# Optimization experiments

Hardware: AMD Instinct MI355X
Metric: run time of the kernel (lower is better)

## Reference

```python
import jax, jax.numpy as jnp
import numpy as np

T, B, D, O = 2048, 32, 512, 512


def setup_inputs() -> dict:
    key = jax.random.key(0)
    ks = jax.random.split(key, 12)
    s = 0.02
    return {
        "word": jax.random.normal(ks[0], (T, B, D), dtype=jnp.float32),
        "Wf": jax.random.normal(ks[1], (D, D), dtype=jnp.float32) * s,
        "bf": jax.random.normal(ks[2], (D,), dtype=jnp.float32) * s,
        "Wi": jax.random.normal(ks[3], (D, D), dtype=jnp.float32) * s,
        "bi": jax.random.normal(ks[4], (D,), dtype=jnp.float32) * s,
        "Wz": jax.random.normal(ks[5], (D, D), dtype=jnp.float32) * s,
        "bz": jax.random.normal(ks[6], (D,), dtype=jnp.float32) * s,
        "Wo": jax.random.normal(ks[7], (D, D), dtype=jnp.float32) * s,
        "bo": jax.random.normal(ks[8], (D,), dtype=jnp.float32) * s,
        "Wy": jax.random.normal(ks[9], (O, D), dtype=jnp.float32) * s,
        "by": jax.random.normal(ks[10], (O,), dtype=jnp.float32) * s,
    }


def reference(word, Wf, bf, Wi, bi, Wz, bz, Wo, bo, Wy, by):
    # Faithful to the original buggy module:
    #  - forward discards the updated cell state, so c == 0 every step and
    #    the zf gate (wf) never affects the output.
    #  - z and zo reuse wi(hidden) instead of wz/wo(hidden).
    #  - the same Linear is applied to letter and hidden, so bias is doubled
    #    in zi (and zf).
    Bsz, Dd = word.shape[1], word.shape[2]

    def step(h, x):  # h: [B, D], x: [B, D]
        hWi = h @ Wi.T                                  # reused by zi, z, zo
        zi = jax.nn.sigmoid(x @ Wi.T + hWi + 2.0 * bi)
        z = jax.nn.sigmoid(x @ Wz.T + bz + hWi + bi)
        zo = jax.nn.sigmoid(x @ Wo.T + bo + hWi + bi)
        c = zi * z                                      # zf * 0 + zi * z
        h_new = zo * jnp.tanh(c)
        return h_new, None

    h0 = jnp.zeros((Bsz, Dd), dtype=word.dtype)
    h_final, _ = jax.lax.scan(step, h0, word)
    # original computes wy(hidden) every step but only returns the last one
    output = h_final @ Wy.T + by                        # [B, O]
    return output
```

## Files before the change

### kernel.cpp

```cpp
#include <hip/hip_runtime.h>

typedef unsigned int u32;
typedef unsigned short u16;
typedef unsigned long long u64;
typedef _Float16 f16;
typedef f16 f16x2 __attribute__((ext_vector_type(2)));

__device__ __forceinline__ float fdot2(u32 a, u32 b, float c) {
#if __has_builtin(__builtin_amdgcn_fdot2)
    return __builtin_amdgcn_fdot2(__builtin_bit_cast(f16x2, a),
                                  __builtin_bit_cast(f16x2, b), c, false);
#else
    f16x2 av = __builtin_bit_cast(f16x2, a), bv = __builtin_bit_cast(f16x2, b);
    c += (float)av[0] * (float)bv[0];
    c += (float)av[1] * (float)bv[1];
    return c;
#endif
}

__device__ __forceinline__ u32 pack2h(float a, float b) {
    f16x2 h; h[0] = (f16)a; h[1] = (f16)b;
    return __builtin_bit_cast(u32, h);
}
__device__ __forceinline__ float h2f(u16 x) { return (float)__builtin_bit_cast(f16, x); }
__device__ __forceinline__ u16 f2h(float x) { f16 h = (f16)x; return __builtin_bit_cast(u16, h); }

__device__ __forceinline__ float fexp(float x) {
#if __has_builtin(__builtin_amdgcn_exp2f)
    return __builtin_amdgcn_exp2f(x * 1.44269504088896f);
#else
    return __expf(x);
#endif
}
__device__ __forceinline__ float frcp(float x) {
#if __has_builtin(__builtin_amdgcn_rcpf)
    return __builtin_amdgcn_rcpf(x);
#else
    return 1.0f / x;
#endif
}
__device__ __forceinline__ float fsigmoid(float x) { return frcp(1.0f + fexp(-x)); }
__device__ __forceinline__ float ftanh_pos(float x) { return 1.0f - 2.0f * frcp(fexp(2.0f * x) + 1.0f); }

__device__ __forceinline__ u64 load_l2(const u64* p) {
    u64 v;
    asm volatile("global_load_dwordx2 %0, %1, off sc0\n\ts_waitcnt vmcnt(0)"
                 : "=v"(v) : "v"(p) : "memory");
    return v;
}
__device__ __forceinline__ void store_l2(u64* p, u64 v) {
    asm volatile("global_store_dwordx2 %0, %1, off sc0" :: "v"(p), "v"(v) : "memory");
}

__global__ __launch_bounds__(256) void k0_pack(const float* __restrict__ Wi,
                                               const float* __restrict__ Wy,
                                               u32* __restrict__ WpkT,
                                               u32* __restrict__ Wypk) {
    const int bx = blockIdx.x, tid = threadIdx.x;
    if (bx < 512) {
        const float2 v = *(const float2*)(Wi + (size_t)bx * 512 + 2 * tid);
        WpkT[(size_t)bx * 256 + tid] = pack2h(v.x, v.y);
    } else {
        const int p = bx - 512;
        #pragma unroll
        for (int r = 0; r < 2; ++r) {
            const int d = tid + 256 * r;
            Wypk[(size_t)p * 512 + d] =
                pack2h(Wy[(size_t)d * 512 + 2 * p], Wy[(size_t)d * 512 + 2 * p + 1]);
        }
    }
}

__global__ __launch_bounds__(256) void k1_gates(
    const float* __restrict__ word,
    const float* __restrict__ Wi, const float* __restrict__ Wz, const float* __restrict__ Wo,
    const float* __restrict__ bi, const float* __restrict__ bz, const float* __restrict__ bo,
    u16* __restrict__ Xi, u16* __restrict__ Xz, u16* __restrict__ Xo)
{
    __shared__ uint4 ws2v[3][128][4];
    __shared__ u32 xs2[2][16][36];

    const int tid = threadIdx.x;
    const int d_l = tid & 63;
    const int bq  = tid >> 6;
    const int t0  = blockIdx.x * 2;
    const int d0  = blockIdx.y * 128;

    const float* Wg[3] = {Wi, Wz, Wo};

    float acc[2][2][8][3];
    #pragma unroll
    for (int tt = 0; tt < 2; ++tt)
        #pragma unroll
        for (int db = 0; db < 2; ++db)
            #pragma unroll
            for (int j = 0; j < 8; ++j)
                #pragma unroll
                for (int g = 0; g < 3; ++g) acc[tt][db][j][g] = 0.0f;

    for (int k0c = 0; k0c < 512; k0c += 32) {
        {
            const int p = tid & 15, bg = tid >> 4;
            #pragma unroll
            for (int tt = 0; tt < 2; ++tt)
                #pragma unroll
                for (int j = 0; j < 2; ++j) {
                    const int bb = bg * 2 + j;
                    const float2 v = *(const float2*)(word + (((size_t)(t0 + tt) * 32 + bb) * 512 + k0c + 2 * p));
                    xs2[tt][p][bb] = pack2h(v.x, v.y);
                }
        }
        {
            #pragma unroll
            for (int cc = 0; cc < 6; ++cc) {
                const int c = tid + 256 * cc;
                const int g = c >> 9, r = c & 511, pg = r >> 7, i = r & 127;
                const float* src = Wg[g] + (size_t)(d0 + i) * 512 + k0c + 8 * pg;
                const float4 v0 = ((const float4*)src)[0];
                const float4 v1 = ((const float4*)src)[1];
                uint4 cell;
                cell.x = pack2h(v0.x, v0.y); cell.y = pack2h(v0.z, v0.w);
                cell.z = pack2h(v1.x, v1.y); cell.w = pack2h(v1.z, v1.w);
                ws2v[g][i][(pg + (i >> 2)) & 3] = cell;
            }
        }
        __syncthreads();
        #pragma unroll
        for (int pg = 0; pg < 4; ++pg) {
            uint4 wc[3][2];
            #pragma unroll
            for (int g = 0; g < 3; ++g)
                #pragma unroll
                for (int db = 0; db < 2; ++db) {
                    const int d = d_l + 64 * db;
                    wc[g][db] = ws2v[g][d][(pg + (d >> 2)) & 3];
                }
            #pragma unroll
            for (int p = 0; p < 4; ++p) {
                const int pair = 4 * pg + p;
                u32 x2[2][8];
                #pragma unroll
                for (int tt = 0; tt < 2; ++tt) {
                    const uint4* xr = (const uint4*)&xs2[tt][pair][bq * 8];
                    uint4 xa = xr[0], xb = xr[1];
                    x2[tt][0] = xa.x; x2[tt][1] = xa.y; x2[tt][2] = xa.z; x2[tt][3] = xa.w;
                    x2[tt][4] = xb.x; x2[tt][5] = xb.y; x2[tt][6] = xb.z; x2[tt][7] = xb.w;
                }
                u32 w[3][2];
                #pragma unroll
                for (int g = 0; g < 3; ++g)
                    #pragma unroll
                    for (int db = 0; db < 2; ++db) {
                        const uint4 v = wc[g][db];
                        w[g][db] = (p == 0) ? v.x : (p == 1) ? v.y : (p == 2) ? v.z : v.w;
                    }
                #pragma unroll
                for (int tt = 0; tt < 2; ++tt)
                    #pragma unroll
                    for (int db = 0; db < 2; ++db)
                        #pragma unroll
                        for (int j = 0; j < 8; ++j)
                            #pragma unroll
                            for (int g = 0; g < 3; ++g)
                                acc[tt][db][j][g] = fdot2(x2[tt][j], w[g][db], acc[tt][db][j][g]);
            }
        }
        __syncthreads();
    }

    #pragma unroll
    for (int db = 0; db < 2; ++db) {
        const int d = d0 + 64 * db + d_l;
        const float b0 = 2.0f * bi[d];
        const float b1 = bz[d] + bi[d];
        const float b2 = bo[d] + bi[d];
        #pragma unroll
        for (int tt = 0; tt < 2; ++tt)
            #pragma unroll
            for (int j = 0; j < 8; ++j) {
                const size_t o = ((size_t)(t0 + tt) * 32 + (bq * 8 + j)) * 512 + d;
                Xi[o] = f2h(acc[tt][db][j][0] + b0);
                Xz[o] = f2h(acc[tt][db][j][1] + b1);
                Xo[o] = f2h(acc[tt][db][j][2] + b2);
            }
    }
}

__global__ __launch_bounds__(512, 2) void k2_recur(
    const u16* __restrict__ Xi, const u16* __restrict__ Xz, const u16* __restrict__ Xo,
    const u32* __restrict__ WpkT, const u32* __restrict__ Wypk,
    u64* __restrict__ exchF, u64* __restrict__ exchS,
    const float* __restrict__ by, float* __restrict__ out)
{
    __shared__ alignas(16) u16 hb[2][256];
    __shared__ alignas(16) u16 hfull[512];

    const int bid  = blockIdx.x;
    const int half = (bid >> 3) & 1;
    const int b    = (bid & 7) | ((bid >> 4) << 3);
    const int tid  = threadIdx.x;

    const uint4* WpkT4 = (const uint4*)WpkT;
    u32 wq[128];
    #pragma unroll
    for (int i = 0; i < 32; ++i) {
        const uint4 v = WpkT4[(size_t)tid * 64 + half * 32 + i];
        wq[4 * i + 0] = v.x; wq[4 * i + 1] = v.y;
        wq[4 * i + 2] = v.z; wq[4 * i + 3] = v.w;
    }
    #pragma unroll
    for (int i = 0; i < 128; ++i) asm volatile("" : "+v"(wq[i]));

    if (tid < 256) hb[0][tid] = (u16)0;
    __syncthreads();

    const size_t me  = (size_t)(b * 2 + half) * 2 * 512 + tid;
    const size_t pa  = (size_t)(b * 2 + (half ^ 1)) * 2 * 512 + tid;
    u64* eoF = exchF + me;  u64* eoS = exchS + me;
    const u64* eiF = exchF + pa;  const u64* eiS = exchS + pa;

    const int ownhalf = ((tid >> 8) == half);
    const int hloc = tid & 255;

    u16 xi_c = Xi[(size_t)b * 512 + tid];
    u16 xz_c = Xz[(size_t)b * 512 + tid];
    u16 xo_c = Xo[(size_t)b * 512 + tid];

    float hn = 0.0f;
    for (int t = 0; t < 2048; ++t) {
        const int par = t & 1;
        const int tn = (t + 1) & 2047;
        const size_t xb = ((size_t)tn * 32 + b) * 512 + tid;
        const u16 xi_n = Xi[xb], xz_n = Xz[xb], xo_n = Xo[xb];

        const uint4* hv = (const uint4*)&hb[par][0];
        float a0 = 0.f, a1 = 0.f, a2 = 0.f, a3 = 0.f;
        #pragma unroll
        for (int i = 0; i < 32; ++i) {
            const uint4 hc = hv[i];
            a0 = fdot2(hc.x, wq[4 * i + 0], a0);
            a1 = fdot2(hc.y, wq[4 * i + 1], a1);
            a2 = fdot2(hc.z, wq[4 * i + 2], a2);
            a3 = fdot2(hc.w, wq[4 * i + 3], a3);
        }
        const float p = (a0 + a1) + (a2 + a3);

        const u32 tag = (u32)(t + 1);
        const u64 msg = ((u64)tag << 32) | (u64)__builtin_bit_cast(u32, p);
        store_l2(eoF + (size_t)par * 512, msg);
        __hip_atomic_store(eoS + (size_t)par * 512, msg,
                           __ATOMIC_RELAXED, __HIP_MEMORY_SCOPE_AGENT);

        u64 m;
        for (;;) {
            m = load_l2(eiF + (size_t)par * 512);
            if ((u32)(m >> 32) == tag) break;
            m = __hip_atomic_load(eiS + (size_t)par * 512,
                                  __ATOMIC_RELAXED, __HIP_MEMORY_SCOPE_AGENT);
            if ((u32)(m >> 32) == tag) break;
        }
        const float v = p + __builtin_bit_cast(float, (u32)m);

        const float zi = fsigmoid(h2f(xi_c) + v);
        const float z  = fsigmoid(h2f(xz_c) + v);
        const float zo = fsigmoid(h2f(xo_c) + v);
        hn = zo * ftanh_pos(zi * z);

        if (ownhalf) hb[par ^ 1][hloc] = f2h(hn);
        __syncthreads();

        xi_c = xi_n; xz_c = xz_n; xo_c = xo_n;
    }

    hfull[tid] = f2h(hn);
    __syncthreads();
    {
        const uint4* hv = (const uint4*)&hfull[0];
        float e0 = 0.f, e1 = 0.f, e2 = 0.f, e3 = 0.f;
        #pragma unroll 8
        for (int i = 0; i < 64; ++i) {
            const uint4 hc = hv[i];
            e0 = fdot2(hc.x, Wypk[(size_t)(4 * i + 0) * 512 + tid], e0);
            e1 = fdot2(hc.y, Wypk[(size_t)(4 * i + 1) * 512 + tid], e1);
            e2 = fdot2(hc.z, Wypk[(size_t)(4 * i + 2) * 512 + tid], e2);
            e3 = fdot2(hc.w, Wypk[(size_t)(4 * i + 3) * 512 + tid], e3);
        }
        out[(size_t)b * 512 + tid] = (e0 + e1) + (e2 + e3) + by[tid];
    }
}

extern "C" void kernel_launch(void* const* d_in, const int* in_sizes, int n_in,
                              void* d_out, int out_size, void* d_ws, size_t ws_size,
                              hipStream_t stream) {
    const float* word = (const float*)d_in[0];
    const float* Wi = (const float*)d_in[3];
    const float* bi = (const float*)d_in[4];
    const float* Wz = (const float*)d_in[5];
    const float* bz = (const float*)d_in[6];
    const float* Wo = (const float*)d_in[7];
    const float* bo = (const float*)d_in[8];
    const float* Wy = (const float*)d_in[9];
    const float* by = (const float*)d_in[10];
    float* out = (float*)d_out;

    char* ws = (char*)d_ws;
    const size_t XN = (size_t)2048 * 32 * 512 * sizeof(u16);
    u16* Xi = (u16*)(ws);
    u16* Xz = (u16*)(ws + XN);
    u16* Xo = (u16*)(ws + 2 * XN);
    u32* WpkT  = (u32*)(ws + 3 * XN);
    u32* Wypk  = (u32*)(ws + 3 * XN + (size_t)524288);
    u64* exchF = (u64*)(ws + 3 * XN + (size_t)2 * 524288);
    u64* exchS = (u64*)(ws + 3 * XN + (size_t)3 * 524288);

    k0_pack<<<768, 256, 0, stream>>>(Wi, Wy, WpkT, Wypk);

    dim3 g1(1024, 4);
    k1_gates<<<g1, 256, 0, stream>>>(word, Wi, Wz, Wo, bi, bz, bo, Xi, Xz, Xo);

    k2_recur<<<64, 512, 0, stream>>>(Xi, Xz, Xo, WpkT, Wypk, exchF, exchS, by, out);
}
```

Baseline: 4.270 ms.

## Merge split recurrence blocks into one 1024-thread block with shared-memory exchange

Each batch element's recurrence now runs in a single 1024-thread workgroup, with the two halves of the K-reduction exchanging partial sums through LDS and barriers. Previously two workgroups on different CUs exchanged them through L2 with tagged spin-polling every timestep. This removes cross-CU global synchronization latency on the serial critical path. The cost is half the CUs in use, an extra barrier per step, and heavy register pressure from 128 weight registers per thread at 1024 threads.

Result: slower. 9.763 ms (+128.6%).

```diff
diff --git a/kernel.cpp b/kernel.cpp
--- a/kernel.cpp
+++ b/kernel.cpp
@@ -41,16 +41,6 @@
 }
 __device__ __forceinline__ float fsigmoid(float x) { return frcp(1.0f + fexp(-x)); }
 __device__ __forceinline__ float ftanh_pos(float x) { return 1.0f - 2.0f * frcp(fexp(2.0f * x) + 1.0f); }
-
-__device__ __forceinline__ u64 load_l2(const u64* p) {
-    u64 v;
-    asm volatile("global_load_dwordx2 %0, %1, off sc0\n\ts_waitcnt vmcnt(0)"
-                 : "=v"(v) : "v"(p) : "memory");
-    return v;
-}
-__device__ __forceinline__ void store_l2(u64* p, u64 v) {
-    asm volatile("global_store_dwordx2 %0, %1, off sc0" :: "v"(p), "v"(v) : "memory");
-}
 
 __global__ __launch_bounds__(256) void k0_pack(const float* __restrict__ Wi,
                                                const float* __restrict__ Wy,
@@ -186,54 +176,52 @@
     }
 }
 
-__global__ __launch_bounds__(512, 2) void k2_recur(
+__global__ __launch_bounds__(1024, 1) void k2_recur(
     const u16* __restrict__ Xi, const u16* __restrict__ Xz, const u16* __restrict__ Xo,
     const u32* __restrict__ WpkT, const u32* __restrict__ Wypk,
-    u64* __restrict__ exchF, u64* __restrict__ exchS,
     const float* __restrict__ by, float* __restrict__ out)
 {
-    __shared__ alignas(16) u16 hb[2][256];
-    __shared__ alignas(16) u16 hfull[512];
-
-    const int bid  = blockIdx.x;
-    const int half = (bid >> 3) & 1;
-    const int b    = (bid & 7) | ((bid >> 4) << 3);
+    __shared__ alignas(16) u16 hb[2][512];
+    __shared__ float pbuf[512];
+
+    const int b    = blockIdx.x;
     const int tid  = threadIdx.x;
+    const int half = tid >> 9;
+    const int d    = tid & 511;
 
     const uint4* WpkT4 = (const uint4*)WpkT;
     u32 wq[128];
     #pragma unroll
     for (int i = 0; i < 32; ++i) {
-        const uint4 v = WpkT4[(size_t)tid * 64 + half * 32 + i];
+        const uint4 v = WpkT4[(size_t)d * 64 + half * 32 + i];
         wq[4 * i + 0] = v.x; wq[4 * i + 1] = v.y;
         wq[4 * i + 2] = v.z; wq[4 * i + 3] = v.w;
     }
     #pragma unroll
     for (int i = 0; i < 128; ++i) asm volatile("" : "+v"(wq[i]));
 
-    if (tid < 256) hb[0][tid] = (u16)0;
+    if (tid < 512) hb[0][tid] = (u16)0;
     __syncthreads();
 
-    const size_t me  = (size_t)(b * 2 + half) * 2 * 512 + tid;
-    const size_t pa  = (size_t)(b * 2 + (half ^ 1)) * 2 * 512 + tid;
-    u64* eoF = exchF + me;  u64* eoS = exchS + me;
-    const u64* eiF = exchF + pa;  const u64* eiS = exchS + pa;
-
-    const int ownhalf = ((tid >> 8) == half);
-    const int hloc = tid & 255;
-
-    u16 xi_c = Xi[(size_t)b * 512 + tid];
-    u16 xz_c = Xz[(size_t)b * 512 + tid];
-    u16 xo_c = Xo[(size_t)b * 512 + tid];
+    u16 xi_c = 0, xz_c = 0, xo_c = 0;
+    if (half == 0) {
+        xi_c = Xi[(size_t)b * 512 + d];
+        xz_c = Xz[(size_t)b * 512 + d];
+        xo_c = Xo[(size_t)b * 512 + d];
+    }
 
     float hn = 0.0f;
     for (int t = 0; t < 2048; ++t) {
         const int par = t & 1;
-        const int tn = (t + 1) & 2047;
-        const size_t xb = ((size_t)tn * 32 + b) * 512 + tid;
-        const u16 xi_n = Xi[xb], xz_n = Xz[xb], xo_n = Xo[xb];
-
-        const uint4* hv = (const uint4*)&hb[par][0];
+
+        u16 xi_n = 0, xz_n = 0, xo_n = 0;
+        if (half == 0) {
+            const int tn = (t + 1) & 2047;
+            const size_t xb = ((size_t)tn * 32 + b) * 512 + d;
+            xi_n = Xi[xb]; xz_n = Xz[xb]; xo_n = Xo[xb];
+        }
+
+        const uint4* hv = (const uint4*)&hb[par][half << 8];
         float a0 = 0.f, a1 = 0.f, a2 = 0.f, a3 = 0.f;
         #pragma unroll
         for (int i = 0; i < 32; ++i) {
@@ -245,47 +233,33 @@
         }
         const float p = (a0 + a1) + (a2 + a3);
 
-        const u32 tag = (u32)(t + 1);
-        const u64 msg = ((u64)tag << 32) | (u64)__builtin_bit_cast(u32, p);
-        store_l2(eoF + (size_t)par * 512, msg);
-        __hip_atomic_store(eoS + (size_t)par * 512, msg,
-                           __ATOMIC_RELAXED, __HIP_MEMORY_SCOPE_AGENT);
-
-        u64 m;
-        for (;;) {
-            m = load_l2(eiF + (size_t)par * 512);
-            if ((u32)(m >> 32) == tag) break;
-            m = __hip_atomic_load(eiS + (size_t)par * 512,
-                                  __ATOMIC_RELAXED, __HIP_MEMORY_SCOPE_AGENT);
-            if ((u32)(m >> 32) == tag) break;
-        }
-        const float v = p + __builtin_bit_cast(float, (u32)m);
-
-        const float zi = fsigmoid(h2f(xi_c) + v);
-        const float z  = fsigmoid(h2f(xz_c) + v);
-        const float zo = fsigmoid(h2f(xo_c) + v);
-        hn = zo * ftanh_pos(zi * z);
-
-        if (ownhalf) hb[par ^ 1][hloc] = f2h(hn);
+        if (half) pbuf[d] = p;
+        __syncthreads();
+        if (!half) {
+            const float v  = p + pbuf[d];
+            const float zi = fsigmoid(h2f(xi_c) + v);
+            const float z  = fsigmoid(h2f(xz_c) + v);
+            const float zo = fsigmoid(h2f(xo_c) + v);
+            hn = zo * ftanh_pos(zi * z);
+            hb[par ^ 1][d] = f2h(hn);
+        }
         __syncthreads();
 
         xi_c = xi_n; xz_c = xz_n; xo_c = xo_n;
     }
 
-    hfull[tid] = f2h(hn);
-    __syncthreads();
-    {
-        const uint4* hv = (const uint4*)&hfull[0];
+    if (half == 0) {
+        const uint4* hv = (const uint4*)&hb[0][0];
         float e0 = 0.f, e1 = 0.f, e2 = 0.f, e3 = 0.f;
         #pragma unroll 8
         for (int i = 0; i < 64; ++i) {
             const uint4 hc = hv[i];
-            e0 = fdot2(hc.x, Wypk[(size_t)(4 * i + 0) * 512 + tid], e0);
-            e1 = fdot2(hc.y, Wypk[(size_t)(4 * i + 1) * 512 + tid], e1);
-            e2 = fdot2(hc.z, Wypk[(size_t)(4 * i + 2) * 512 + tid], e2);
-            e3 = fdot2(hc.w, Wypk[(size_t)(4 * i + 3) * 512 + tid], e3);
-        }
-        out[(size_t)b * 512 + tid] = (e0 + e1) + (e2 + e3) + by[tid];
+            e0 = fdot2(hc.x, Wypk[(size_t)(4 * i + 0) * 512 + d], e0);
+            e1 = fdot2(hc.y, Wypk[(size_t)(4 * i + 1) * 512 + d], e1);
+            e2 = fdot2(hc.z, Wypk[(size_t)(4 * i + 2) * 512 + d], e2);
+            e3 = fdot2(hc.w, Wypk[(size_t)(4 * i + 3) * 512 + d], e3);
+        }
+        out[(size_t)b * 512 + d] = (e0 + e1) + (e2 + e3) + by[d];
     }
 }
 
@@ -308,15 +282,13 @@
     u16* Xi = (u16*)(ws);
     u16* Xz = (u16*)(ws + XN);
     u16* Xo = (u16*)(ws + 2 * XN);
-    u32* WpkT  = (u32*)(ws + 3 * XN);
-    u32* Wypk  = (u32*)(ws + 3 * XN + (size_t)524288);
-    u64* exchF = (u64*)(ws + 3 * XN + (size_t)2 * 524288);
-    u64* exchS = (u64*)(ws + 3 * XN + (size_t)3 * 524288);
+    u32* WpkT = (u32*)(ws + 3 * XN);
+    u32* Wypk = (u32*)(ws + 3 * XN + (size_t)524288);
 
     k0_pack<<<768, 256, 0, stream>>>(Wi, Wy, WpkT, Wypk);
 
     dim3 g1(1024, 4);
     k1_gates<<<g1, 256, 0, stream>>>(word, Wi, Wz, Wo, bi, bz, bo, Xi, Xz, Xo);
 
-    k2_recur<<<64, 512, 0, stream>>>(Xi, Xz, Xo, WpkT, Wypk, exchF, exchS, by, out);
-}
+    k2_recur<<<32, 1024, 0, stream>>>(Xi, Xz, Xo, WpkT, Wypk, by, out);
+}
```
